# Performance work log

Hardware: AMD Instinct MI355X
Metric: run time of the kernel (lower is better)

The kernel has to match this reference:

```python
import jax, jax.numpy as jnp
import numpy as np

D_MODEL = 96
D_INNER = 192        # expand_factor * d_model
D_STATE = 16
DT_RANK = 6          # ceil(d_model / 16)
D_CONV = 4
N_LAYERS = 2
EPS = 1e-5


def conv3d(x, w, b=None, padding=((0, 0), (0, 0), (0, 0)), groups=1):
    # x: (N, C, L, H, W), w: (O, C//groups, kL, kH, kW)
    y = jax.lax.conv_general_dilated(
        x, w, window_strides=(1, 1, 1), padding=padding,
        dimension_numbers=('NCDHW', 'OIDHW', 'NCDHW'),
        feature_group_count=groups)
    return y if b is None else y + b[None, :, None, None, None]


def rmsnorm(x, w):
    # faithful to source: mean of squares over the LAST dim (W)
    return x * jax.lax.rsqrt(jnp.mean(x * x, axis=-1, keepdims=True) + EPS) * w


def mamba_block(x, p):
    # x: (N, d_model, L, H, W)
    L = x.shape[2]
    xz = conv3d(x, p['in_proj_w'], padding=((0, 0), (1, 1), (1, 1)))
    xi, z = xz[:, :D_INNER], xz[:, D_INNER:]
    # causal depthwise temporal conv: pad d_conv-1, crop to L
    xi = conv3d(xi, p['conv1d_w'], p['conv1d_b'],
                padding=((D_CONV - 1, D_CONV - 1), (0, 0), (0, 0)),
                groups=D_INNER)[:, :, :L]
    xi = jax.nn.silu(xi)
    # --- SSM (selective scan, pscan path) ---
    A = -jnp.exp(p['A_log'])                                   # (K, S)
    dbc = conv3d(xi, p['x_proj_w'])                            # (N, dt_rank+2S, L, H, W)
    delta = jax.nn.softplus(conv3d(dbc[:, :DT_RANK], p['dt_proj_w'], p['dt_proj_b']))  # (N, K, L, H, W)
    B = jnp.moveaxis(dbc[:, DT_RANK:DT_RANK + D_STATE], 1, -1)  # (N, L, H, W, S)
    C = dbc[:, DT_RANK + D_STATE:]                              # (N, S, L, H, W)
    deltaA = jnp.exp(delta[..., None] * A[None, :, None, None, None, :])  # (N,K,L,H,W,S)
    BX = delta[..., None] * B[:, None] * xi[..., None]                    # (N,K,L,H,W,S)

    def op(e1, e2):
        a1, b1 = e1
        a2, b2 = e2
        return a1 * a2, a2 * b1 + b2

    _, hs = jax.lax.associative_scan(op, (deltaA, BX), axis=2)  # scan over L
    y = jnp.einsum('nklhws,nslhw->nklhw', hs, C) + p['D'][None, :, None, None, None] * xi
    out = y * jax.nn.silu(z)
    return conv3d(out, p['out_proj_w'])


def _forward(x, in_proj_w, conv1d_w, conv1d_b, x_proj_w, dt_proj_w,
             dt_proj_b, A_log, D, out_proj_w, norm_w):
    for l in range(N_LAYERS):
        p = dict(in_proj_w=in_proj_w[l], conv1d_w=conv1d_w[l], conv1d_b=conv1d_b[l],
                 x_proj_w=x_proj_w[l], dt_proj_w=dt_proj_w[l], dt_proj_b=dt_proj_b[l],
                 A_log=A_log[l], D=D[l], out_proj_w=out_proj_w[l], norm_w=norm_w[l])
        x = mamba_block(rmsnorm(x, p['norm_w']), p) + x   # ResidualBlock
        x = x[:, :, 0:1]                                   # Mamba.forward keeps t=0 only
    return x


def setup_inputs() -> dict:
    key = jax.random.key(0)
    ks = jax.random.split(key, 12)
    Lk = N_LAYERS
    x = jax.random.normal(ks[0], (2, D_MODEL, 8, 24, 24), dtype=jnp.float32)
    in_proj_w = jax.random.normal(ks[1], (Lk, 2 * D_INNER, D_MODEL, 1, 3, 3), jnp.float32) * (D_MODEL * 9) ** -0.5
    conv1d_w = jax.random.normal(ks[2], (Lk, D_INNER, 1, D_CONV, 1, 1), jnp.float32) * D_CONV ** -0.5
    conv1d_b = jax.random.normal(ks[3], (Lk, D_INNER), jnp.float32) * 0.02
    x_proj_w = jax.random.normal(ks[4], (Lk, DT_RANK + 2 * D_STATE, D_INNER, 1, 1, 1), jnp.float32) * D_INNER ** -0.5
    dt_std = DT_RANK ** -0.5
    dt_proj_w = jax.random.uniform(ks[5], (Lk, D_INNER, DT_RANK, 1, 1, 1), jnp.float32, -dt_std, dt_std)
    # dt bias init: inv softplus of dt ~ LogUniform(dt_min, dt_max)
    dt = jnp.exp(jax.random.uniform(ks[6], (Lk, D_INNER), jnp.float32)
                 * (np.log(0.1) - np.log(0.001)) + np.log(0.001))
    dt = jnp.clip(dt, 1e-4, None)
    dt_proj_b = dt + jnp.log(-jnp.expm1(-dt))
    A_log = jnp.log(jnp.tile(jnp.arange(1, D_STATE + 1, dtype=jnp.float32), (Lk, D_INNER, 1)))
    D = jnp.ones((Lk, D_INNER), jnp.float32)
    out_proj_w = jax.random.normal(ks[7], (Lk, D_MODEL, D_INNER, 1, 1, 1), jnp.float32) * D_INNER ** -0.5
    norm_w = jnp.ones((Lk, 1, D_MODEL, 1, 1, 1), jnp.float32)
    return {'x': x, 'in_proj_w': in_proj_w, 'conv1d_w': conv1d_w, 'conv1d_b': conv1d_b,
            'x_proj_w': x_proj_w, 'dt_proj_w': dt_proj_w, 'dt_proj_b': dt_proj_b,
            'A_log': A_log, 'D': D, 'out_proj_w': out_proj_w, 'norm_w': norm_w}


def reference(x, in_proj_w, conv1d_w, conv1d_b, x_proj_w, dt_proj_w,
              dt_proj_b, A_log, D, out_proj_w, norm_w):
    return _forward(x, in_proj_w, conv1d_w, conv1d_b, x_proj_w, dt_proj_w,
                    dt_proj_b, A_log, D, out_proj_w, norm_w)
```

## Files before the change

kernel.cpp:

```cpp
#include <hip/hip_runtime.h>
#include <math.h>

#define NB   2
#define CM   96
#define CI   192
#define CO   384
#define HP   24
#define WP   24
#define PX   576
#define DTR  6
#define NDBC 38
#define CSPLIT 8
#define CCH  12

__device__ __forceinline__ float siluf(float x){ return x / (1.f + expf(-x)); }
__device__ __forceinline__ float softplusf(float x){ return x > 20.f ? x : log1pf(expf(x)); }
__device__ __forceinline__ unsigned short f2bf(float f){
    unsigned u = __float_as_uint(f);
    return (unsigned short)((u + 0x7fffu + ((u >> 16) & 1u)) >> 16);
}
__device__ __forceinline__ float bflo(unsigned u){ return __uint_as_float(u << 16); }
__device__ __forceinline__ float bfhi(unsigned u){ return __uint_as_float(u & 0xffff0000u); }

#define NW_IN (2*CO*CM*9)
#define WQB_L (CM*CO*8)
#define WRB_L (CM*CO)
#define WPT_L (CI*CM)
__global__ void prep_k(const float* __restrict__ ipw, const float* __restrict__ opw,
                       unsigned short* __restrict__ wQb, unsigned short* __restrict__ wRb,
                       float* __restrict__ wpT){
    int idx = blockIdx.x*256 + threadIdx.x;
    if (idx < NW_IN){
        int l = idx / (CO*CM*9);
        int r = idx % (CO*CM*9);
        int o = r / (CM*9);
        int r2 = r % (CM*9);
        int c = r2 / 9;
        int k = r2 % 9;
        unsigned short v = f2bf(ipw[idx]);
        if (k < 8) wQb[(long)l*WQB_L + ((c*CO + o)<<3) + k] = v;
        else       wRb[(long)l*WRB_L + c*CO + o] = v;
    } else {
        int j = idx - NW_IN;
        if (j < 2*CI*CM){
            int l = j / (CI*CM);
            int r = j % (CI*CM);
            int c = r / CM;
            int m = r % CM;
            wpT[l*WPT_L + c*CM + m] = opw[(l*CM + m)*CI + c];
        }
    }
}

__global__ __launch_bounds__(256, 3) void conv_k(
    const float* __restrict__ x, long nStr, long cStr,
    const float* __restrict__ nw,
    const unsigned short* __restrict__ wQb, const unsigned short* __restrict__ wRb,
    float* __restrict__ acc)
{
    __shared__ float hs[CCH][3][28];
    __shared__ float scl[CCH][3];
    int bx  = blockIdx.x;
    int og2 = blockIdx.y;
    int cs  = blockIdx.z;
    int n  = bx / HP, hh = bx % HP;
    int tid = threadIdx.x;
    int c0 = cs*CCH;

    if (tid < CCH*3){
        int c = tid/3, j = tid%3;
        int row = hh + j - 1;
        float s = 0.f;
        if (row >= 0 && row < HP){
            const float4* xp4 = (const float4*)(x + (long)n*nStr + (long)(c0+c)*cStr + row*WP);
            #pragma unroll
            for (int w4 = 0; w4 < WP/4; w4++){
                float4 v = xp4[w4];
                s += v.x*v.x + v.y*v.y + v.z*v.z + v.w*v.w;
            }
            s = rsqrtf(s*(1.0f/WP) + 1e-5f) * nw[c0+c];
        }
        scl[c][j] = s;
    }
    __syncthreads();

    for (int idx = tid; idx < CCH*3*28; idx += 256){
        int c = idx/84; int rem = idx%84; int j = rem/28; int wc = rem%28;
        int row = hh + j - 1;
        float v = 0.f;
        if (row >= 0 && row < HP && wc >= 1 && wc <= WP)
            v = x[(long)n*nStr + (long)(c0+c)*cStr + row*WP + (wc-1)] * scl[c][j];
        hs[c][j][wc] = v;
    }
    __syncthreads();

    int ol = tid & 63;
    int obase = og2*192 + ol;
    int x0 = (tid >> 6) * 6;
    float a0[3][6] = {{0,0,0,0,0,0},{0,0,0,0,0,0},{0,0,0,0,0,0}};
    const uint4* wq4 = (const uint4*)wQb;

    uint4 nw4[3]; unsigned short nw8[3];
    float2 nh[3][4];
    {
        int cg = c0;
        #pragma unroll
        for (int oc = 0; oc < 3; oc++){
            nw4[oc] = wq4[cg*CO + obase + oc*64];
            nw8[oc] = wRb[cg*CO + obase + oc*64];
        }
        #pragma unroll
        for (int j = 0; j < 3; j++)
            #pragma unroll
            for (int i = 0; i < 4; i++)
                nh[j][i] = *(const float2*)(&hs[0][j][x0] + 2*i);
    }

    for (int c = 0; c < CCH; c++){
        uint4 cw4[3]; unsigned short cw8[3]; float2 ch[3][4];
        #pragma unroll
        for (int oc = 0; oc < 3; oc++){ cw4[oc] = nw4[oc]; cw8[oc] = nw8[oc]; }
        #pragma unroll
        for (int j = 0; j < 3; j++)
            #pragma unroll
            for (int i = 0; i < 4; i++) ch[j][i] = nh[j][i];

        if (c + 1 < CCH){
            int cg = c0 + c + 1;
            #pragma unroll
            for (int oc = 0; oc < 3; oc++){
                nw4[oc] = wq4[cg*CO + obase + oc*64];
                nw8[oc] = wRb[cg*CO + obase + oc*64];
            }
            #pragma unroll
            for (int j = 0; j < 3; j++)
                #pragma unroll
                for (int i = 0; i < 4; i++)
                    nh[j][i] = *(const float2*)(&hs[c+1][j][x0] + 2*i);
        }

        float r0v[8], r1v[8], r2v[8];
        #pragma unroll
        for (int i = 0; i < 4; i++){
            r0v[2*i] = ch[0][i].x; r0v[2*i+1] = ch[0][i].y;
            r1v[2*i] = ch[1][i].x; r1v[2*i+1] = ch[1][i].y;
            r2v[2*i] = ch[2][i].x; r2v[2*i+1] = ch[2][i].y;
        }
        #pragma unroll
        for (int oc = 0; oc < 3; oc++){
            uint4 wv = cw4[oc];
            float w0 = bflo(wv.x), w1 = bfhi(wv.x);
            float w2 = bflo(wv.y), w3 = bfhi(wv.y);
            float w4 = bflo(wv.z), w5 = bfhi(wv.z);
            float w6 = bflo(wv.w), w7 = bfhi(wv.w);
            float w8 = bflo((unsigned)cw8[oc]);
            #pragma unroll
            for (int p = 0; p < 6; p++){
                a0[oc][p] += w0*r0v[p] + w1*r0v[p+1] + w2*r0v[p+2]
                           + w3*r1v[p] + w4*r1v[p+1] + w5*r1v[p+2]
                           + w6*r2v[p] + w7*r2v[p+1] + w8*r2v[p+2];
            }
        }
    }

    #pragma unroll
    for (int oc = 0; oc < 3; oc++){
        float* ap = acc + ((long)(cs*NB + n)*PX + hh*WP + x0)*CO + obase + oc*64;
        #pragma unroll
        for (int p = 0; p < 6; p++) ap[p*CO] = a0[oc][p];
    }
}

__global__ __launch_bounds__(256) void ssmproj_k(
    const float* __restrict__ acc,
    const float* __restrict__ c1w, const float* __restrict__ c1b,
    const float* __restrict__ xpw, const float* __restrict__ dtw,
    const float* __restrict__ dtb, const float* __restrict__ Dp,
    const float* __restrict__ wpT,
    const float* __restrict__ xres, long nStrR, long cStrR,
    float* __restrict__ dst)
{
    __shared__ float gl[4][CI];
    int wave = threadIdx.x >> 6, lane = threadIdx.x & 63;
    int p0 = blockIdx.x*4;
    int p  = p0 + wave;
    int n  = p / PX, px = p % PX;

    float xi[3], sz[3];
    #pragma unroll
    for (int t = 0; t < 3; t++){
        int c = lane + 64*t;
        float xr = 0.f, zr = 0.f;
        #pragma unroll
        for (int q = 0; q < CSPLIT; q++){
            const float* ap = acc + ((long)(q*NB + n)*PX + px)*CO;
            xr += ap[c]; zr += ap[CI + c];
        }
        xi[t] = siluf(xr*c1w[c*4 + 3] + c1b[c]);
        sz[t] = siluf(zr);
    }

    float dbc[NDBC];
    #pragma unroll
    for (int j = 0; j < NDBC; j++){
        float s = 0.f;
        #pragma unroll
        for (int t = 0; t < 3; t++) s += xi[t]*xpw[j*CI + lane + 64*t];
        dbc[j] = s;
    }
    #pragma unroll
    for (int step = 1; step < 64; step <<= 1){
        #pragma unroll
        for (int j = 0; j < NDBC; j++) dbc[j] += __shfl_xor(dbc[j], step, 64);
    }
    float BC = 0.f;
    #pragma unroll
    for (int s = 0; s < 16; s++) BC += dbc[6+s]*dbc[22+s];

    #pragma unroll
    for (int t = 0; t < 3; t++){
        int c = lane + 64*t;
        float dl = dtb[c];
        #pragma unroll
        for (int r = 0; r < DTR; r++) dl += dbc[r]*dtw[c*DTR + r];
        dl = softplusf(dl);
        gl[wave][c] = xi[t]*(dl*BC + Dp[c])*sz[t];
    }
    __syncthreads();

    for (int idx = threadIdx.x; idx < 4*CM; idx += 256){
        int pl = idx / CM, m = idx % CM;
        int pp = p0 + pl;
        int nn = pp / PX, ppx = pp % PX;
        const float* g = gl[pl];
        float s0 = 0.f, s1 = 0.f, s2 = 0.f, s3 = 0.f;
        for (int c = 0; c < CI; c += 4){
            s0 += g[c+0]*wpT[(c+0)*CM + m];
            s1 += g[c+1]*wpT[(c+1)*CM + m];
            s2 += g[c+2]*wpT[(c+2)*CM + m];
            s3 += g[c+3]*wpT[(c+3)*CM + m];
        }
        float s = (s0+s1) + (s2+s3);
        s += xres[(long)nn*nStrR + (long)m*cStrR + ppx];
        dst[(nn*CM + m)*PX + ppx] = s;
    }
}

extern "C" void kernel_launch(void* const* d_in, const int* in_sizes, int n_in,
                              void* d_out, int out_size, void* d_ws, size_t ws_size,
                              hipStream_t stream) {
    const float* x_in = (const float*)d_in[0];
    const float* ipw  = (const float*)d_in[1];
    const float* c1w  = (const float*)d_in[2];
    const float* c1b  = (const float*)d_in[3];
    const float* xpw  = (const float*)d_in[4];
    const float* dtw  = (const float*)d_in[5];
    const float* dtb  = (const float*)d_in[6];
    const float* Dp   = (const float*)d_in[8];
    const float* opw  = (const float*)d_in[9];
    const float* nw   = (const float*)d_in[10];

    char* ws = (char*)d_ws;
    unsigned short* wQb = (unsigned short*)ws;
    unsigned short* wRb = wQb + 2*WQB_L;
    float* wpT = (float*)(wRb + 2*WRB_L);
    float* acc = wpT + 2*WPT_L;
    float* x1  = acc + (long)CSPLIT*NB*PX*CO;

    prep_k<<<(NW_IN + 2*CI*CM + 255)/256, 256, 0, stream>>>(ipw, opw, wQb, wRb, wpT);

    conv_k<<<dim3(NB*HP, 2, CSPLIT), 256, 0, stream>>>(
        x_in, 96L*8*PX, 8L*PX, nw, wQb, wRb, acc);
    ssmproj_k<<<NB*PX/4, 256, 0, stream>>>(
        acc, c1w, c1b, xpw, dtw, dtb, Dp, wpT,
        x_in, 96L*8*PX, 8L*PX, x1);

    conv_k<<<dim3(NB*HP, 2, CSPLIT), 256, 0, stream>>>(
        x1, 96L*PX, (long)PX, nw + CM, wQb + WQB_L, wRb + WRB_L, acc);
    ssmproj_k<<<NB*PX/4, 256, 0, stream>>>(
        acc, c1w + CI*4, c1b + CI, xpw + NDBC*CI, dtw + CI*DTR, dtb + CI, Dp + CI, wpT + WPT_L,
        x1, 96L*PX, (long)PX, (float*)d_out);
}
```

Baseline: 151.9 us.

## Overlap layer-2 weight preparation with layer-1 conv via extra grid slice

The weight conversion kernel now only prepares layer-1 weights (bf16 in_proj repack and out_proj transpose). Layer-2 weight preparation is folded into the first conv launch as an extra z-slice of blocks that run alongside the conv blocks. This shortens the serial prep kernel ahead of the first conv and hides the layer-2 conversion under conv work. The cost is extra blocks competing for CUs in the first conv launch.

```diff
diff --git a/kernel.cpp b/kernel.cpp
--- a/kernel.cpp
+++ b/kernel.cpp
@@ -12,6 +12,11 @@
 #define NDBC 38
 #define CSPLIT 8
 #define CCH  12
+#define IPW_L (CO*CM*9)
+#define WQB_L (CM*CO*8)
+#define WRB_L (CM*CO)
+#define WPT_L (CI*CM)
+#define NPREP (IPW_L + WPT_L)
 
 __device__ __forceinline__ float siluf(float x){ return x / (1.f + expf(-x)); }
 __device__ __forceinline__ float softplusf(float x){ return x > 20.f ? x : log1pf(expf(x)); }
@@ -22,49 +27,57 @@
 __device__ __forceinline__ float bflo(unsigned u){ return __uint_as_float(u << 16); }
 __device__ __forceinline__ float bfhi(unsigned u){ return __uint_as_float(u & 0xffff0000u); }
 
-#define NW_IN (2*CO*CM*9)
-#define WQB_L (CM*CO*8)
-#define WRB_L (CM*CO)
-#define WPT_L (CI*CM)
-__global__ void prep_k(const float* __restrict__ ipw, const float* __restrict__ opw,
-                       unsigned short* __restrict__ wQb, unsigned short* __restrict__ wRb,
-                       float* __restrict__ wpT){
-    int idx = blockIdx.x*256 + threadIdx.x;
-    if (idx < NW_IN){
-        int l = idx / (CO*CM*9);
-        int r = idx % (CO*CM*9);
-        int o = r / (CM*9);
-        int r2 = r % (CM*9);
+__device__ __forceinline__ void prep_elem(
+    int idx, const float* __restrict__ ipw, const float* __restrict__ opw,
+    unsigned short* __restrict__ wQb, unsigned short* __restrict__ wRb,
+    float* __restrict__ wpT)
+{
+    if (idx < IPW_L){
+        int o = idx / (CM*9);
+        int r2 = idx % (CM*9);
         int c = r2 / 9;
         int k = r2 % 9;
         unsigned short v = f2bf(ipw[idx]);
-        if (k < 8) wQb[(long)l*WQB_L + ((c*CO + o)<<3) + k] = v;
-        else       wRb[(long)l*WRB_L + c*CO + o] = v;
+        if (k < 8) wQb[((c*CO + o)<<3) + k] = v;
+        else       wRb[c*CO + o] = v;
     } else {
-        int j = idx - NW_IN;
-        if (j < 2*CI*CM){
-            int l = j / (CI*CM);
-            int r = j % (CI*CM);
-            int c = r / CM;
-            int m = r % CM;
-            wpT[l*WPT_L + c*CM + m] = opw[(l*CM + m)*CI + c];
-        }
-    }
+        int j = idx - IPW_L;
+        int c = j / CM, m = j % CM;
+        wpT[c*CM + m] = opw[(long)m*CI + c];
+    }
+}
+
+__global__ void prep1_k(const float* __restrict__ ipw, const float* __restrict__ opw,
+                        unsigned short* __restrict__ wQb, unsigned short* __restrict__ wRb,
+                        float* __restrict__ wpT){
+    int idx = blockIdx.x*256 + threadIdx.x;
+    if (idx < NPREP) prep_elem(idx, ipw, opw, wQb, wRb, wpT);
 }
 
 __global__ __launch_bounds__(256, 3) void conv_k(
     const float* __restrict__ x, long nStr, long cStr,
     const float* __restrict__ nw,
     const unsigned short* __restrict__ wQb, const unsigned short* __restrict__ wRb,
-    float* __restrict__ acc)
+    float* __restrict__ acc,
+    const float* __restrict__ ipw1, const float* __restrict__ opw1,
+    unsigned short* __restrict__ wQb1, unsigned short* __restrict__ wRb1,
+    float* __restrict__ wpT1)
 {
     __shared__ float hs[CCH][3][28];
     __shared__ float scl[CCH][3];
     int bx  = blockIdx.x;
     int og2 = blockIdx.y;
     int cs  = blockIdx.z;
+    int tid = threadIdx.x;
+
+    if (cs == CSPLIT){
+        int base = (bx + NB*HP*og2)*256 + tid;
+        for (int idx = base; idx < NPREP; idx += NB*HP*2*256)
+            prep_elem(idx, ipw1, opw1, wQb1, wRb1, wpT1);
+        return;
+    }
+
     int n  = bx / HP, hh = bx % HP;
-    int tid = threadIdx.x;
     int c0 = cs*CCH;
 
     if (tid < CCH*3){
@@ -267,16 +280,18 @@
     float* acc = wpT + 2*WPT_L;
     float* x1  = acc + (long)CSPLIT*NB*PX*CO;
 
-    prep_k<<<(NW_IN + 2*CI*CM + 255)/256, 256, 0, stream>>>(ipw, opw, wQb, wRb, wpT);
-
-    conv_k<<<dim3(NB*HP, 2, CSPLIT), 256, 0, stream>>>(
-        x_in, 96L*8*PX, 8L*PX, nw, wQb, wRb, acc);
+    prep1_k<<<(NPREP + 255)/256, 256, 0, stream>>>(ipw, opw, wQb, wRb, wpT);
+
+    conv_k<<<dim3(NB*HP, 2, CSPLIT+1), 256, 0, stream>>>(
+        x_in, 96L*8*PX, 8L*PX, nw, wQb, wRb, acc,
+        ipw + IPW_L, opw + CM*CI, wQb + WQB_L, wRb + WRB_L, wpT + WPT_L);
     ssmproj_k<<<NB*PX/4, 256, 0, stream>>>(
         acc, c1w, c1b, xpw, dtw, dtb, Dp, wpT,
         x_in, 96L*8*PX, 8L*PX, x1);
 
     conv_k<<<dim3(NB*HP, 2, CSPLIT), 256, 0, stream>>>(
-        x1, 96L*PX, (long)PX, nw + CM, wQb + WQB_L, wRb + WRB_L, acc);
+        x1, 96L*PX, (long)PX, nw + CM, wQb + WQB_L, wRb + WRB_L, acc,
+        nullptr, nullptr, nullptr, nullptr, nullptr);
     ssmproj_k<<<NB*PX/4, 256, 0, stream>>>(
         acc, c1w + CI*4, c1b + CI, xpw + NDBC*CI, dtw + CI*DTR, dtb + CI, Dp + CI, wpT + WPT_L,
         x1, 96L*PX, (long)PX, (float*)d_out);
```

After: 150.9 us, median of 2. Within noise of the previous version (-0.6%).
